# Performance work log

Measured on AMD Instinct MI355X. Metric: run time of the kernel, lower is better.

The kernel has to match this reference:

```python
import jax, jax.numpy as jnp
import numpy as np
import math

B, C, SEG, SEGLEN, K, GROUPS, WG = 8, 256, 40, 200, 10, 32, 4
L4 = SEGLEN // 4            # 50 temporal slots per segment
N = SEG * L4                # 2000 total points
WIDTH = GROUPS * WG         # 128 bottleneck width


def build_neighbor_idx(seg_lens):
    """Exact numpy replication of torch get_temporal_graph's neighbor-list loop.
    Returns flat (into B*N rows) neighbor indices of shape (B, N, 3)."""
    seg_lens = np.asarray(seg_lens)
    Bn, S = seg_lens.shape
    nb = np.zeros((Bn, S * L4, 3), dtype=np.int64)
    for i in range(Bn):
        last_valid = 0
        skip_seg = 0
        base = i * S * L4
        for j in range(S):
            valid = math.ceil(seg_lens[i, j] / 4.0)
            for k in range(L4):
                idx = j * L4 + k
                if k < valid:
                    nb[i, idx] = [base + last_valid, base + idx, base + idx]
                    last_valid = idx
                    if k == 0 and j != 0:
                        nb[i, skip_seg, 2] = base + idx
                    if k == valid - 1:
                        skip_seg = idx
                    else:
                        nb[i, idx, 2] = base + idx + 1
                else:
                    nb[i, idx] = [base + idx] * 3
    return nb


def conv1x1(x, W, b):
    # x: (B, Cin, N, T), W: (Cout, Cin)
    return jnp.einsum('bcnt,oc->bont', x, W) + b[None, :, None, None]


def grouped_1x3(x, W, b):
    # x: (B, WIDTH, N, 3), W: (WIDTH, WIDTH//GROUPS, 3); valid conv -> T_out = 1
    Bn, _, Nn, _ = x.shape
    xg = x.reshape(Bn, GROUPS, WIDTH // GROUPS, Nn, 3)
    Wg = W.reshape(GROUPS, WIDTH // GROUPS, WIDTH // GROUPS, 3)
    y = jnp.einsum('bgcnt,goct->bgon', xg, Wg)
    return y.reshape(Bn, WIDTH, Nn, 1) + b[None, :, None, None]


def grouped_1x1(x, W, b):
    # x: (B, WIDTH, N, T), W: (WIDTH, WIDTH//GROUPS)
    Bn, _, Nn, T = x.shape
    xg = x.reshape(Bn, GROUPS, WIDTH // GROUPS, Nn, T)
    Wg = W.reshape(GROUPS, WIDTH // GROUPS, WIDTH // GROUPS)
    y = jnp.einsum('bgcnt,goc->bgont', xg, Wg)
    return y.reshape(Bn, WIDTH, Nn, T) + b[None, :, None, None]


def setup_inputs() -> dict:
    key = jax.random.key(0)
    ks = jax.random.split(key, 10)
    s = 0.05
    x = jax.random.normal(ks[0], (B, C, N), dtype=jnp.float32)
    seg_lens = jax.random.randint(ks[1], (B, SEG), 0, 201)
    neighbor_idx = jnp.asarray(build_neighbor_idx(np.asarray(seg_lens)))
    return dict(
        x=x, seg_lens=seg_lens, neighbor_idx=neighbor_idx,
        tW1=jax.random.normal(ks[2], (WIDTH, C), jnp.float32) * s,
        tb1=jnp.zeros((WIDTH,), jnp.float32),
        tW2=jax.random.normal(ks[3], (WIDTH, WIDTH // GROUPS, 3), jnp.float32) * s,
        tb2=jnp.zeros((WIDTH,), jnp.float32),
        tW3=jax.random.normal(ks[4], (C, WIDTH), jnp.float32) * s,
        tb3=jnp.zeros((C,), jnp.float32),
        sW1=jax.random.normal(ks[5], (WIDTH, 2 * C), jnp.float32) * s,
        sb1=jnp.zeros((WIDTH,), jnp.float32),
        sW2=jax.random.normal(ks[6], (WIDTH, WIDTH // GROUPS), jnp.float32) * s,
        sb2=jnp.zeros((WIDTH,), jnp.float32),
        sW3=jax.random.normal(ks[7], (C, WIDTH), jnp.float32) * s,
        sb3=jnp.zeros((C,), jnp.float32),
    )


def reference(x, seg_lens, neighbor_idx, tW1, tb1, tW2, tb2, tW3, tb3,
              sW1, sb1, sW2, sb2, sW3, sb3):
    relu = jax.nn.relu
    B_, C_, N_ = x.shape
    flat = x.transpose(0, 2, 1).reshape(B_ * N_, C_)  # (B*N, C)

    # --- temporal branch: gather 3 temporal-graph neighbors -> (B, C, N, 3) ---
    tg = flat[neighbor_idx.reshape(-1)].reshape(B_, N_, 3, C_).transpose(0, 3, 1, 2)
    h = relu(conv1x1(tg, tW1, tb1))
    h = relu(grouped_1x3(h, tW2, tb2))
    tout = conv1x1(h, tW3, tb3).max(axis=-1)  # (B, C, N)

    # --- semantic branch: kNN graph feature (style=1) ---
    xx = jnp.sum(x * x, axis=1)                       # (B, N)
    inner = jnp.einsum('bci,bcj->bij', x, x)          # (B, N, N)
    pd = 2.0 * inner - xx[:, None, :] - xx[:, :, None]  # negative sq. distances
    _, idx = jax.lax.top_k(pd, K)                     # (B, N, K)
    base = (jnp.arange(B_) * N_)[:, None, None]
    nbr = flat[(idx + base).reshape(-1)].reshape(B_, N_, K, C_)
    center = jnp.broadcast_to(x.transpose(0, 2, 1)[:, :, None, :], (B_, N_, K, C_))
    xf = jnp.concatenate([nbr, center], axis=3).transpose(0, 3, 1, 2)  # (B, 2C, N, K)
    g = relu(conv1x1(xf, sW1, sb1))
    g = relu(grouped_1x1(g, sW2, sb2))
    sout = conv1x1(g, sW3, sb3).max(axis=-1)  # (B, C, N)

    return relu(tout + x + sout)
```

## Files before the change

kernel.cpp:

```cpp
#include <hip/hip_runtime.h>

#define NPTS 2000
#define NBATCH 8
#define NC 256
#define NW 128
#define NK 10
#define NROWS (NBATCH * NPTS)
#define JPAD 2048

typedef _Float16 f16x8 __attribute__((ext_vector_type(8)));
typedef _Float16 f16x4 __attribute__((ext_vector_type(4)));
typedef float f32x4 __attribute__((ext_vector_type(4)));

__device__ __forceinline__ float dot4(float4 a, float4 b) {
    return a.x*b.x + a.y*b.y + a.z*b.z + a.w*b.w;
}
__device__ __forceinline__ float4 relu4(float4 a) {
    return make_float4(fmaxf(a.x,0.f), fmaxf(a.y,0.f), fmaxf(a.z,0.f), fmaxf(a.w,0.f));
}
__device__ __forceinline__ float4 add4(float4 a, float4 b) {
    return make_float4(a.x+b.x, a.y+b.y, a.z+b.z, a.w+b.w);
}

__device__ __forceinline__ void ins10(float d, int j, float* vals, int* idxs) {
    if (d > vals[9]) {
        float v = d; int id = j;
        #pragma unroll
        for (int s = 0; s < 10; ++s) {
            if (v > vals[s]) {
                float tv = vals[s]; vals[s] = v; v = tv;
                int   ti = idxs[s]; idxs[s] = id; id = ti;
            }
        }
    }
}

__device__ __forceinline__ void gl_lds16(const void* g, void* l) {
    __builtin_amdgcn_global_load_lds(
        (const __attribute__((address_space(1))) void*)g,
        (__attribute__((address_space(3))) void*)l, 16, 0, 0);
}

__global__ __launch_bounds__(256) void k_prep(
    const float* __restrict__ x, _Float16* __restrict__ xb,
    float* __restrict__ xx)
{
    __shared__ float T[64][259];
    __shared__ float Pp[64][4];
    const int t  = threadIdx.x;
    const int b  = blockIdx.x >> 5;
    const int n0 = (blockIdx.x & 31) * 64;

    #pragma unroll
    for (int p = 0; p < 64; ++p) {
        const int idx = p*256 + t;
        const int c = idx >> 6, nl = idx & 63;
        T[nl][c] = x[((size_t)b*NC + c)*NPTS + min(n0 + nl, NPTS-1)];
    }
    __syncthreads();

    const int row = t & 63, q = t >> 6;
    const int gr  = n0 + row;
    const bool ok = gr < NPTS;
    const int sx  = gr & 7;
    float ss = 0.f;
    #pragma unroll
    for (int u = 0; u < 2; ++u) {
        const int kc = 2*q + u;
        const size_t base = ((size_t)(b*8 + kc)*JPAD + gr) * 64;
        #pragma unroll
        for (int g = 0; g < 4; ++g) {
            f16x8 vh, vl;
            #pragma unroll
            for (int e = 0; e < 8; ++e) {
                const float f = ok ? T[row][kc*32 + g*8 + e] : 0.f;
                ss = fmaf(f, f, ss);
                const _Float16 h = (_Float16)f;
                vh[e] = h;
                vl[e] = (_Float16)(f - (float)h);
            }
            *(f16x8*)&xb[base + (size_t)((g     ^ sx))*8] = vh;
            *(f16x8*)&xb[base + (size_t)(((4|g) ^ sx))*8] = vl;
        }
    }
    Pp[row][q] = ss;
    __syncthreads();
    if (t < 64 && n0 + t < NPTS)
        xx[(size_t)b*NPTS + n0 + t] = Pp[t][0] + Pp[t][1] + Pp[t][2] + Pp[t][3];
}

__global__ __launch_bounds__(256) void k_wprep(const float* __restrict__ a,
                                               _Float16* __restrict__ o, int n)
{
    const int i = (blockIdx.x*256 + threadIdx.x)*4;
    if (i < n) {
        const float4 v = *(const float4*)&a[i];
        f16x4 h = {(_Float16)v.x, (_Float16)v.y, (_Float16)v.z, (_Float16)v.w};
        *(f16x4*)&o[i] = h;
    }
}

__global__ __launch_bounds__(256) void k_wcat(
    const float* __restrict__ tW1, const float* __restrict__ sW1,
    _Float16* __restrict__ whcat)
{
    const int idx = blockIdx.x*256 + threadIdx.x;
    const int n = idx >> 8, k = idx & 255;
    float v;
    if (n < 128)      v = tW1[n*256 + k];
    else if (n < 256) v = sW1[(n-128)*512 + k];
    else              v = sW1[(n-256)*512 + 256 + k];
    whcat[idx] = (_Float16)v;
}

__global__ __launch_bounds__(256) void k_rowmm(
    const _Float16* __restrict__ xb, const _Float16* __restrict__ whcat,
    const float* __restrict__ tb1, const float* __restrict__ sb1,
    float* __restrict__ T1r, float* __restrict__ P, float* __restrict__ Q)
{
    const int t = threadIdx.x, lane = t & 63, w = t >> 6;
    const int lr = lane & 15, rg = lane >> 4;
    const int r0 = blockIdx.x * 16;
    const int b  = r0 / NPTS, jr = r0 % NPTS;

    const int row = jr + lr;
    const int sx  = row & 7;
    f16x8 ah[8], al[8];
    #pragma unroll
    for (int kc = 0; kc < 8; ++kc) {
        const size_t base = ((size_t)(b*8 + kc)*JPAD + row) * 64;
        ah[kc] = *(const f16x8*)&xb[base + (size_t)((rg     ^ sx))*8];
        al[kc] = *(const f16x8*)&xb[base + (size_t)(((4|rg) ^ sx))*8];
    }

    #pragma unroll
    for (int nt = 0; nt < 6; ++nt) {
        const int n0 = (w*6 + nt) * 16;
        f32x4 acc = {0.f,0.f,0.f,0.f};
        #pragma unroll
        for (int kc = 0; kc < 8; ++kc) {
            const f16x8 bw = *(const f16x8*)&whcat[(size_t)(n0 + lr)*256 + kc*32 + rg*8];
            acc = __builtin_amdgcn_mfma_f32_16x16x32_f16(ah[kc], bw, acc, 0,0,0);
            acc = __builtin_amdgcn_mfma_f32_16x16x32_f16(al[kc], bw, acc, 0,0,0);
        }
        const int n = n0 + lr;
        float bias; bool dorelu; float* dst;
        if (n < 128)      { bias = tb1[n];     dorelu = true;  dst = T1r + (size_t)r0*NW + n; }
        else if (n < 256) { bias = 0.f;        dorelu = false; dst = P   + (size_t)r0*NW + (n-128); }
        else              { bias = sb1[n-256]; dorelu = false; dst = Q   + (size_t)r0*NW + (n-256); }
        #pragma unroll
        for (int q = 0; q < 4; ++q) {
            float v = acc[q] + bias;
            if (dorelu) v = fmaxf(v, 0.f);
            dst[(size_t)(rg*4 + q)*NW] = v;
        }
    }
}

__global__ __attribute__((amdgpu_flat_work_group_size(256,256), amdgpu_waves_per_eu(2,2)))
void k_dist(const _Float16* __restrict__ xb, const float* __restrict__ xx,
            float* __restrict__ pval, int* __restrict__ pidx)
{
    __shared__ __align__(16) char smem[65536];

    const int t    = threadIdx.x;
    const int b    = blockIdx.x & 7;
    const int ip   = (blockIdx.x >> 3) & 15;
    const int jp   = blockIdx.x >> 7;
    const int i0   = ip * 128;
    const int j0p  = jp * 128;
    const int lane = t & 63;
    const int w    = t >> 6;
    const int lr   = lane & 15, rg = lane >> 4;
    const char* xbb = (const char*)xb;
    const float* xxb = xx + (size_t)b * NPTS;

    f32x4 acc[2][8] = {};

    {
        const size_t gbase = (size_t)(b*8 + 0) * JPAD;
        const char* gi = xbb + (gbase + i0) * 128;
        const char* gj = xbb + (gbase + j0p) * 128;
        #pragma unroll
        for (int r2 = 0; r2 < 4; ++r2) {
            gl_lds16(gi + t*16 + r2*4096, smem + t*16 + r2*4096);
            gl_lds16(gj + t*16 + r2*4096, smem + 16384 + t*16 + r2*4096);
        }
    }
    __syncthreads();

    for (int kc = 0; kc < 8; ++kc) {
        const int buf = kc & 1;

        if (kc < 7) {
            const size_t gbase = (size_t)(b*8 + kc + 1) * JPAD;
            const char* gi = xbb + (gbase + i0) * 128;
            const char* gj = xbb + (gbase + j0p) * 128;
            char* li = smem + (buf ^ 1)*32768;
            #pragma unroll
            for (int r2 = 0; r2 < 4; ++r2) {
                gl_lds16(gi + t*16 + r2*4096, li + t*16 + r2*4096);
                gl_lds16(gj + t*16 + r2*4096, li + 16384 + t*16 + r2*4096);
            }
        }

        {
            const char* IB = smem + buf*32768;
            const char* JB = IB + 16384;
            f16x8 bhf[2], blf[2];
            #pragma unroll
            for (int it = 0; it < 2; ++it) {
                const int il = (w*2 + it)*16 + lr;
                const int sx = il & 7;
                bhf[it] = *(const f16x8*)(IB + il*128 + ((rg     ^ sx))*16);
                blf[it] = *(const f16x8*)(IB + il*128 + (((4|rg) ^ sx))*16);
            }
            #pragma unroll
            for (int jt = 0; jt < 8; ++jt) {
                const int jl = jt*16 + lr;
                const int sx = jl & 7;
                const f16x8 ajh = *(const f16x8*)(JB + jl*128 + ((rg     ^ sx))*16);
                const f16x8 ajl = *(const f16x8*)(JB + jl*128 + (((4|rg) ^ sx))*16);
                #pragma unroll
                for (int it = 0; it < 2; ++it) {
                    acc[it][jt] = __builtin_amdgcn_mfma_f32_16x16x32_f16(ajh, bhf[it], acc[it][jt], 0,0,0);
                    acc[it][jt] = __builtin_amdgcn_mfma_f32_16x16x32_f16(ajh, blf[it], acc[it][jt], 0,0,0);
                    acc[it][jt] = __builtin_amdgcn_mfma_f32_16x16x32_f16(ajl, bhf[it], acc[it][jt], 0,0,0);
                }
            }
        }
        __syncthreads();
    }

    float v0[10], v1[10]; int x0[10], x1[10];
    #pragma unroll
    for (int s = 0; s < 10; ++s) { v0[s]=v1[s]=-3.0e38f; x0[s]=x1[s]=0x7fffffff; }

    #pragma unroll
    for (int jt = 0; jt < 8; ++jt) {
        const int jg0 = j0p + jt*16 + rg*4;
        const f32x4 xv = *(const f32x4*)&xxb[min(jg0, NPTS-4)];
        {
            const float d0 = 2.f*acc[0][jt][0] - xv[0];
            const float d1 = 2.f*acc[0][jt][1] - xv[1];
            const float d2 = 2.f*acc[0][jt][2] - xv[2];
            const float d3 = 2.f*acc[0][jt][3] - xv[3];
            if (fmaxf(fmaxf(d0,d1), fmaxf(d2,d3)) > v0[9]) {
                if (jg0     < NPTS) ins10(d0, jg0,     v0, x0);
                if (jg0 + 1 < NPTS) ins10(d1, jg0 + 1, v0, x0);
                if (jg0 + 2 < NPTS) ins10(d2, jg0 + 2, v0, x0);
                if (jg0 + 3 < NPTS) ins10(d3, jg0 + 3, v0, x0);
            }
        }
        {
            const float d0 = 2.f*acc[1][jt][0] - xv[0];
            const float d1 = 2.f*acc[1][jt][1] - xv[1];
            const float d2 = 2.f*acc[1][jt][2] - xv[2];
            const float d3 = 2.f*acc[1][jt][3] - xv[3];
            if (fmaxf(fmaxf(d0,d1), fmaxf(d2,d3)) > v1[9]) {
                if (jg0     < NPTS) ins10(d0, jg0,     v1, x1);
                if (jg0 + 1 < NPTS) ins10(d1, jg0 + 1, v1, x1);
                if (jg0 + 2 < NPTS) ins10(d2, jg0 + 2, v1, x1);
                if (jg0 + 3 < NPTS) ins10(d3, jg0 + 3, v1, x1);
            }
        }
    }

    float* mval = (float*)smem;
    int*   midx = (int*)(smem + 20480);
    {
        const int g0 = (w*2 + 0)*16 + lr;
        const int g1 = (w*2 + 1)*16 + lr;
        #pragma unroll
        for (int s = 0; s < 10; ++s) {
            mval[(g0*4 + rg)*10 + s] = v0[s];  midx[(g0*4 + rg)*10 + s] = x0[s];
            mval[(g1*4 + rg)*10 + s] = v1[s];  midx[(g1*4 + rg)*10 + s] = x1[s];
        }
    }
    __syncthreads();
    {
        const int g = t >> 1, pr = t & 1;
        float* va = &mval[(g*4 + pr)*10];     int* ia = &midx[(g*4 + pr)*10];
        const float* vb = &mval[(g*4 + pr + 2)*10]; const int* ib = &midx[(g*4 + pr + 2)*10];
        float ov[10]; int oi[10]; int pa = 0, pb = 0;
        #pragma unroll
        for (int s = 0; s < 10; ++s) {
            const float A = va[pa], Bv = vb[pb];
            const int  Ai = ia[pa], Bi = ib[pb];
            const bool ta = (A > Bv) || (A == Bv && Ai < Bi);
            ov[s] = ta ? A : Bv; oi[s] = ta ? Ai : Bi;
            pa += ta ? 1 : 0; pb += ta ? 0 : 1;
        }
        #pragma unroll
        for (int s = 0; s < 10; ++s) { va[s] = ov[s]; ia[s] = oi[s]; }
    }
    __syncthreads();
    if (t < 128) {
        const int g = t;
        const int ig = i0 + g;
        if (ig < NPTS) {
            const float* va = &mval[(g*4 + 0)*10]; const int* ia = &midx[(g*4 + 0)*10];
            const float* vb = &mval[(g*4 + 1)*10]; const int* ib = &midx[(g*4 + 1)*10];
            float* ov = &pval[((size_t)(b*NPTS + ig)*16 + jp)*10];
            int*   oi = &pidx[((size_t)(b*NPTS + ig)*16 + jp)*10];
            int pa = 0, pb = 0;
            #pragma unroll
            for (int s = 0; s < 10; ++s) {
                const float A = va[pa], Bv = vb[pb];
                const int  Ai = ia[pa], Bi = ib[pb];
                const bool ta = (A > Bv) || (A == Bv && Ai < Bi);
                ov[s] = ta ? A : Bv; oi[s] = ta ? Ai : Bi;
                pa += ta ? 1 : 0; pb += ta ? 0 : 1;
            }
        }
    }
}

__global__ __launch_bounds__(256) void k_tkm1(
    const float* __restrict__ pval, const int* __restrict__ pidx,
    float* __restrict__ pval2, int* __restrict__ pidx2)
{
    const int idx = blockIdx.x*256 + threadIdx.x;
    if (idx >= NROWS*4) return;
    const int r = idx >> 2, qt = idx & 3;
    const float* v  = &pval[((size_t)r*16 + qt*4)*10];
    const int*   ix = &pidx[((size_t)r*16 + qt*4)*10];
    float* ov = &pval2[(size_t)idx*10];
    int*   oi = &pidx2[(size_t)idx*10];
    int p0 = 0, p1 = 0, p2 = 0, p3 = 0;
    #pragma unroll
    for (int s = 0; s < NK; ++s) {
        float bv = -3.4e38f; int bi = 0x7fffffff; int bl = 0;
        { const float vv = v[p0];      const int ii = ix[p0];
          if (vv > bv || (vv == bv && ii < bi)) { bv = vv; bi = ii; bl = 0; } }
        { const float vv = v[10 + p1]; const int ii = ix[10 + p1];
          if (vv > bv || (vv == bv && ii < bi)) { bv = vv; bi = ii; bl = 1; } }
        { const float vv = v[20 + p2]; const int ii = ix[20 + p2];
          if (vv > bv || (vv == bv && ii < bi)) { bv = vv; bi = ii; bl = 2; } }
        { const float vv = v[30 + p3]; const int ii = ix[30 + p3];
          if (vv > bv || (vv == bv && ii < bi)) { bv = vv; bi = ii; bl = 3; } }
        p0 += (bl == 0); p1 += (bl == 1); p2 += (bl == 2); p3 += (bl == 3);
        ov[s] = bv; oi[s] = bi;
    }
}

__global__ __launch_bounds__(256) void k_tkm2(
    const float* __restrict__ pval2, const int* __restrict__ pidx2,
    int* __restrict__ tk)
{
    const int r = blockIdx.x*256 + threadIdx.x;
    if (r >= NROWS) return;
    const float* v  = &pval2[(size_t)r*40];
    const int*   ix = &pidx2[(size_t)r*40];
    const int base = (r / NPTS) * NPTS;
    int* op = &tk[(size_t)r*NK];
    int p0 = 0, p1 = 0, p2 = 0, p3 = 0;
    #pragma unroll
    for (int s = 0; s < NK; ++s) {
        float bv = -3.4e38f; int bi = 0x7fffffff; int bl = 0;
        { const float vv = v[p0];      const int ii = ix[p0];
          if (vv > bv || (vv == bv && ii < bi)) { bv = vv; bi = ii; bl = 0; } }
        { const float vv = v[10 + p1]; const int ii = ix[10 + p1];
          if (vv > bv || (vv == bv && ii < bi)) { bv = vv; bi = ii; bl = 1; } }
        { const float vv = v[20 + p2]; const int ii = ix[20 + p2];
          if (vv > bv || (vv == bv && ii < bi)) { bv = vv; bi = ii; bl = 2; } }
        { const float vv = v[30 + p3]; const int ii = ix[30 + p3];
          if (vv > bv || (vv == bv && ii < bi)) { bv = vv; bi = ii; bl = 3; } }
        p0 += (bl == 0); p1 += (bl == 1); p2 += (bl == 2); p3 += (bl == 3);
        op[s] = base + bi;
    }
}

#define AST 136
__global__ __launch_bounds__(256, 2) void k_fused(
    const float* __restrict__ x,
    const int* __restrict__ nb, const int* __restrict__ tk,
    const float* __restrict__ T1r, const float* __restrict__ P, const float* __restrict__ Q,
    const float* __restrict__ tW2, const float* __restrict__ tb2,
    const float* __restrict__ sW2, const float* __restrict__ sb2,
    const _Float16* __restrict__ wt3h, const _Float16* __restrict__ ws3h,
    const float* __restrict__ tb3, const float* __restrict__ sb3,
    float* __restrict__ out)
{
    __shared__ __align__(16) _Float16 A16[144*AST];
    __shared__ float Ssm[8][260];
    __shared__ float Zr[8][260];

    const int t  = threadIdx.x;
    const int r0 = blockIdx.x * 8;
    const int bb = r0 / NPTS;
    const int n0 = r0 % NPTS;

    {
        const float4 z4 = make_float4(0.f,0.f,0.f,0.f);
        float4* p4 = (float4*)A16;
        #pragma unroll
        for (int i = 0; i < 10; ++i) {
            const int idx = t + i*256;
            if (idx < 2448) p4[idx] = z4;
        }
    }
    __syncthreads();

    {
        const int o    = t & 127;
        const int half = t >> 7;
        const int g4   = o & ~3;

        const float4 f0 = *(const float4*)&tW2[o*12];
        const float4 f1 = *(const float4*)&tW2[o*12 + 4];
        const float4 f2 = *(const float4*)&tW2[o*12 + 8];
        const float4 wt0 = make_float4(f0.x, f0.w, f1.z, f2.y);
        const float4 wt1 = make_float4(f0.y, f1.x, f1.w, f2.z);
        const float4 wt2 = make_float4(f0.z, f1.y, f2.x, f2.w);
        const float4 wsw = *(const float4*)&sW2[o*4];
        const float tb2o = tb2[o], sb2o = sb2[o];

        #pragma unroll
        for (int ptl = 0; ptl < 4; ++ptl) {
            const int pt = half*4 + ptl;
            const int r  = r0 + pt;
            const int nb0 = nb[r*3+0], nb1 = nb[r*3+1], nb2 = nb[r*3+2];
            int ki[NK];
            #pragma unroll
            for (int k = 0; k < NK; ++k) ki[k] = tk[r*NK + k];
            const float4 h0 = *(const float4*)&T1r[(size_t)nb0*NW + g4];
            const float4 h1 = *(const float4*)&T1r[(size_t)nb1*NW + g4];
            const float4 h2 = *(const float4*)&T1r[(size_t)nb2*NW + g4];
            const float4 qf = *(const float4*)&Q[(size_t)r*NW + g4];
            float4 pf[NK];
            #pragma unroll
            for (int k = 0; k < NK; ++k) pf[k] = *(const float4*)&P[(size_t)ki[k]*NW + g4];

            const float z = tb2o + dot4(wt0,h0) + dot4(wt1,h1) + dot4(wt2,h2);
            A16[(128 + pt)*AST + o] = (_Float16)fmaxf(z, 0.f);
            #pragma unroll
            for (int k = 0; k < NK; ++k) {
                const float4 g1 = relu4(add4(pf[k], qf));
                A16[(pt*16 + k)*AST + o] = (_Float16)fmaxf(dot4(wsw, g1) + sb2o, 0.f);
            }
        }
    }
    __syncthreads();

    const int lane = t & 63, w = t >> 6;
    const int lr = lane & 15, lg = lane >> 4;
    const int n0w = w * 64;

    f32x4 accG[8][4] = {};
    f32x4 accZ[4] = {};

    #pragma unroll
    for (int kt = 0; kt < 4; ++kt) {
        const int ko = kt*32 + lg*8;
        f16x8 bs[4], bt[4];
        #pragma unroll
        for (int nt = 0; nt < 4; ++nt) {
            const int n = n0w + nt*16 + lr;
            bs[nt] = *(const f16x8*)&ws3h[n*NW + ko];
            bt[nt] = *(const f16x8*)&wt3h[n*NW + ko];
        }
        #pragma unroll
        for (int mt = 0; mt < 8; ++mt) {
            const f16x8 a = *(const f16x8*)&A16[(mt*16 + lr)*AST + ko];
            #pragma unroll
            for (int nt = 0; nt < 4; ++nt)
                accG[mt][nt] = __builtin_amdgcn_mfma_f32_16x16x32_f16(a, bs[nt], accG[mt][nt], 0,0,0);
        }
        const f16x8 az = *(const f16x8*)&A16[(128 + lr)*AST + ko];
        #pragma unroll
        for (int nt = 0; nt < 4; ++nt)
            accZ[nt] = __builtin_amdgcn_mfma_f32_16x16x32_f16(az, bt[nt], accZ[nt], 0,0,0);
    }

    const int rg = lg;
    #pragma unroll
    for (int mt = 0; mt < 8; ++mt) {
        #pragma unroll
        for (int nt = 0; nt < 4; ++nt) {
            float v;
            if (rg < 2)       v = fmaxf(fmaxf(accG[mt][nt][0], accG[mt][nt][1]),
                                        fmaxf(accG[mt][nt][2], accG[mt][nt][3]));
            else if (rg == 2) v = fmaxf(accG[mt][nt][0], accG[mt][nt][1]);
            else              v = -3.0e38f;
            v = fmaxf(v, __shfl_xor(v, 16));
            v = fmaxf(v, __shfl_xor(v, 32));
            if (lane < 16) Ssm[mt][n0w + nt*16 + lane] = v;
        }
    }
    #pragma unroll
    for (int nt = 0; nt < 4; ++nt) {
        #pragma unroll
        for (int q = 0; q < 4; ++q) {
            if (rg < 2) Zr[rg*4 + q][n0w + nt*16 + lr] = accZ[nt][q];
        }
    }
    __syncthreads();

    {
        const int c = t;
        const float tb = tb3[c], sb = sb3[c];
        const size_t go = ((size_t)bb*NC + c)*NPTS + n0;
        const float4 xv0 = *(const float4*)&x[go];
        const float4 xv1 = *(const float4*)&x[go + 4];
        const float xr[8] = {xv0.x,xv0.y,xv0.z,xv0.w, xv1.x,xv1.y,xv1.z,xv1.w};
        float ov[8];
        #pragma unroll
        for (int p = 0; p < 8; ++p)
            ov[p] = fmaxf(Zr[p][c] + tb + Ssm[p][c] + sb + xr[p], 0.f);
        *(float4*)&out[go]     = make_float4(ov[0],ov[1],ov[2],ov[3]);
        *(float4*)&out[go + 4] = make_float4(ov[4],ov[5],ov[6],ov[7]);
    }
}

extern "C" void kernel_launch(void* const* d_in, const int* in_sizes, int n_in,
                              void* d_out, int out_size, void* d_ws, size_t ws_size,
                              hipStream_t stream) {
    (void)in_sizes; (void)n_in; (void)out_size; (void)ws_size;
    const float* x   = (const float*)d_in[0];
    const int*   nb  = (const int*)d_in[2];
    const float* tW1 = (const float*)d_in[3];
    const float* tb1 = (const float*)d_in[4];
    const float* tW2 = (const float*)d_in[5];
    const float* tb2 = (const float*)d_in[6];
    const float* tW3 = (const float*)d_in[7];
    const float* tb3 = (const float*)d_in[8];
    const float* sW1 = (const float*)d_in[9];
    const float* sb1 = (const float*)d_in[10];
    const float* sW2 = (const float*)d_in[11];
    const float* sb2 = (const float*)d_in[12];
    const float* sW3 = (const float*)d_in[13];
    const float* sb3 = (const float*)d_in[14];
    float* out = (float*)d_out;

    float* ws  = (float*)d_ws;
    float* T1r   = ws;
    float* P     = ws + 2048000;
    float* Q     = ws + 4096000;
    float* xxp   = ws + 6144000;
    int*   tk    = (int*)(ws + 6160000);
    float* pval  = ws + 6320000;
    int*   pidx  = (int*)(ws + 8880000);
    float* pval2 = ws + 11440000;
    int*   pidx2 = (int*)(ws + 12080000);
    _Float16* xb    = (_Float16*)(ws + 12720000);
    _Float16* whcat = xb + (size_t)NBATCH * 8 * JPAD * 64;
    _Float16* wt3h  = whcat + 384 * 256;
    _Float16* ws3h  = wt3h + NC * NW;

    k_prep<<<NBATCH * 32, 256, 0, stream>>>(x, xb, xxp);
    k_wcat<<<384, 256, 0, stream>>>(tW1, sW1, whcat);
    k_wprep<<<32, 256, 0, stream>>>(tW3, wt3h, NC * NW);
    k_wprep<<<32, 256, 0, stream>>>(sW3, ws3h, NC * NW);
    k_rowmm<<<NROWS / 16, 256, 0, stream>>>(xb, whcat, tb1, sb1, T1r, P, Q);
    k_dist<<<2048, 256, 0, stream>>>(xb, xxp, pval, pidx);
    k_tkm1<<<(NROWS*4 + 255) / 256, 256, 0, stream>>>(pval, pidx, pval2, pidx2);
    k_tkm2<<<(NROWS + 255) / 256, 256, 0, stream>>>(pval2, pidx2, tk);
    k_fused<<<NROWS / 8, 256, 0, stream>>>(x, nb, tk, T1r, P, Q,
                                           tW2, tb2, sW2, sb2, wt3h, ws3h, tb3, sb3, out);
}
```

Before: 390.9 us.

## Stage distance tile through LDS and run top-10 selection per row-half

The k_dist epilogue now writes MFMA accumulators to a padded LDS buffer and reads them back so each thread scans 32 contiguous columns of one row. Previously each thread held two sets of 10-entry top-k lists in registers across the scattered MFMA output layout. The xx norms are also staged in LDS. This is meant to cut register pressure from the two live top-10 lists and give a more regular selection scan, at the cost of extra LDS traffic and several more block barriers. The launch attribute changes to __launch_bounds__(256, 2).

Measured after the change: 390.8 us. About the same (-0.0%).

```diff
diff --git a/kernel.cpp b/kernel.cpp
--- a/kernel.cpp
+++ b/kernel.cpp
@@ -157,11 +157,12 @@
     }
 }
 
-__global__ __attribute__((amdgpu_flat_work_group_size(256,256), amdgpu_waves_per_eu(2,2)))
+__global__ __launch_bounds__(256, 2)
 void k_dist(const _Float16* __restrict__ xb, const float* __restrict__ xx,
             float* __restrict__ pval, int* __restrict__ pidx)
 {
-    __shared__ __align__(16) char smem[65536];
+    __shared__ __align__(16) char smem[66048];
+    float* xxs = (float*)(smem + 65536);
 
     const int t    = threadIdx.x;
     const int b    = blockIdx.x & 7;
@@ -173,7 +174,8 @@
     const int w    = t >> 6;
     const int lr   = lane & 15, rg = lane >> 4;
     const char* xbb = (const char*)xb;
-    const float* xxb = xx + (size_t)b * NPTS;
+
+    if (t < 128) xxs[t] = xx[(size_t)b*NPTS + min(j0p + t, NPTS-1)];
 
     f32x4 acc[2][8] = {};
 
@@ -232,78 +234,54 @@
         __syncthreads();
     }
 
-    float v0[10], v1[10]; int x0[10], x1[10];
-    #pragma unroll
-    for (int s = 0; s < 10; ++s) { v0[s]=v1[s]=-3.0e38f; x0[s]=x1[s]=0x7fffffff; }
-
-    #pragma unroll
-    for (int jt = 0; jt < 8; ++jt) {
-        const int jg0 = j0p + jt*16 + rg*4;
-        const f32x4 xv = *(const f32x4*)&xxb[min(jg0, NPTS-4)];
+    float* Sbuf = (float*)smem;
+    float* mval = (float*)(smem + 34816);
+    int*   midx = (int*)(smem + 45056);
+
+    #pragma unroll
+    for (int it = 0; it < 2; ++it) {
+        #pragma unroll
+        for (int jt = 0; jt < 8; ++jt)
+            *(f32x4*)&Sbuf[(w*16 + lr)*132 + jt*16 + rg*4] = acc[it][jt];
+        __syncthreads();
+
+        float vv[10]; int xi[10];
+        #pragma unroll
+        for (int s = 0; s < 10; ++s) { vv[s] = -3.0e38f; xi[s] = 0x7fffffff; }
         {
-            const float d0 = 2.f*acc[0][jt][0] - xv[0];
-            const float d1 = 2.f*acc[0][jt][1] - xv[1];
-            const float d2 = 2.f*acc[0][jt][2] - xv[2];
-            const float d3 = 2.f*acc[0][jt][3] - xv[3];
-            if (fmaxf(fmaxf(d0,d1), fmaxf(d2,d3)) > v0[9]) {
-                if (jg0     < NPTS) ins10(d0, jg0,     v0, x0);
-                if (jg0 + 1 < NPTS) ins10(d1, jg0 + 1, v0, x0);
-                if (jg0 + 2 < NPTS) ins10(d2, jg0 + 2, v0, x0);
-                if (jg0 + 3 < NPTS) ins10(d3, jg0 + 3, v0, x0);
-            }
-        }
+            const int row = t & 63, jc = t >> 6;
+            const float* srow = &Sbuf[row*132 + jc*32];
+            #pragma unroll
+            for (int e4 = 0; e4 < 8; ++e4) {
+                const int jl = jc*32 + e4*4;
+                const int jg = j0p + jl;
+                const f32x4 sv = *(const f32x4*)&srow[e4*4];
+                const f32x4 xv = *(const f32x4*)&xxs[jl];
+                const float d0 = 2.f*sv[0] - xv[0];
+                const float d1 = 2.f*sv[1] - xv[1];
+                const float d2 = 2.f*sv[2] - xv[2];
+                const float d3 = 2.f*sv[3] - xv[3];
+                if (fmaxf(fmaxf(d0,d1), fmaxf(d2,d3)) > vv[9]) {
+                    if (jg     < NPTS) ins10(d0, jg,     vv, xi);
+                    if (jg + 1 < NPTS) ins10(d1, jg + 1, vv, xi);
+                    if (jg + 2 < NPTS) ins10(d2, jg + 2, vv, xi);
+                    if (jg + 3 < NPTS) ins10(d3, jg + 3, vv, xi);
+                }
+            }
+        }
+        __syncthreads();
         {
-            const float d0 = 2.f*acc[1][jt][0] - xv[0];
-            const float d1 = 2.f*acc[1][jt][1] - xv[1];
-            const float d2 = 2.f*acc[1][jt][2] - xv[2];
-            const float d3 = 2.f*acc[1][jt][3] - xv[3];
-            if (fmaxf(fmaxf(d0,d1), fmaxf(d2,d3)) > v1[9]) {
-                if (jg0     < NPTS) ins10(d0, jg0,     v1, x1);
-                if (jg0 + 1 < NPTS) ins10(d1, jg0 + 1, v1, x1);
-                if (jg0 + 2 < NPTS) ins10(d2, jg0 + 2, v1, x1);
-                if (jg0 + 3 < NPTS) ins10(d3, jg0 + 3, v1, x1);
-            }
-        }
-    }
-
-    float* mval = (float*)smem;
-    int*   midx = (int*)(smem + 20480);
-    {
-        const int g0 = (w*2 + 0)*16 + lr;
-        const int g1 = (w*2 + 1)*16 + lr;
-        #pragma unroll
-        for (int s = 0; s < 10; ++s) {
-            mval[(g0*4 + rg)*10 + s] = v0[s];  midx[(g0*4 + rg)*10 + s] = x0[s];
-            mval[(g1*4 + rg)*10 + s] = v1[s];  midx[(g1*4 + rg)*10 + s] = x1[s];
-        }
-    }
-    __syncthreads();
-    {
-        const int g = t >> 1, pr = t & 1;
-        float* va = &mval[(g*4 + pr)*10];     int* ia = &midx[(g*4 + pr)*10];
-        const float* vb = &mval[(g*4 + pr + 2)*10]; const int* ib = &midx[(g*4 + pr + 2)*10];
-        float ov[10]; int oi[10]; int pa = 0, pb = 0;
-        #pragma unroll
-        for (int s = 0; s < 10; ++s) {
-            const float A = va[pa], Bv = vb[pb];
-            const int  Ai = ia[pa], Bi = ib[pb];
-            const bool ta = (A > Bv) || (A == Bv && Ai < Bi);
-            ov[s] = ta ? A : Bv; oi[s] = ta ? Ai : Bi;
-            pa += ta ? 1 : 0; pb += ta ? 0 : 1;
-        }
-        #pragma unroll
-        for (int s = 0; s < 10; ++s) { va[s] = ov[s]; ia[s] = oi[s]; }
-    }
-    __syncthreads();
-    if (t < 128) {
-        const int g = t;
-        const int ig = i0 + g;
-        if (ig < NPTS) {
-            const float* va = &mval[(g*4 + 0)*10]; const int* ia = &midx[(g*4 + 0)*10];
-            const float* vb = &mval[(g*4 + 1)*10]; const int* ib = &midx[(g*4 + 1)*10];
-            float* ov = &pval[((size_t)(b*NPTS + ig)*16 + jp)*10];
-            int*   oi = &pidx[((size_t)(b*NPTS + ig)*16 + jp)*10];
-            int pa = 0, pb = 0;
+            const int row = t & 63, jc = t >> 6;
+            const int base = (row*4 + jc)*10;
+            #pragma unroll
+            for (int s = 0; s < 10; ++s) { mval[base+s] = vv[s]; midx[base+s] = xi[s]; }
+        }
+        __syncthreads();
+        if (t < 128) {
+            const int g = t >> 1, pr = t & 1;
+            float* va = &mval[(g*4 + pr)*10];     int* ia = &midx[(g*4 + pr)*10];
+            const float* vb = &mval[(g*4 + pr + 2)*10]; const int* ib = &midx[(g*4 + pr + 2)*10];
+            float ov[10]; int oi[10]; int pa = 0, pb = 0;
             #pragma unroll
             for (int s = 0; s < 10; ++s) {
                 const float A = va[pa], Bv = vb[pb];
@@ -312,7 +290,30 @@
                 ov[s] = ta ? A : Bv; oi[s] = ta ? Ai : Bi;
                 pa += ta ? 1 : 0; pb += ta ? 0 : 1;
             }
-        }
+            #pragma unroll
+            for (int s = 0; s < 10; ++s) { va[s] = ov[s]; ia[s] = oi[s]; }
+        }
+        __syncthreads();
+        if (t < 64) {
+            const int g = t;
+            const int ig = i0 + (g >> 4)*32 + it*16 + (g & 15);
+            if (ig < NPTS) {
+                const float* va = &mval[(g*4 + 0)*10]; const int* ia = &midx[(g*4 + 0)*10];
+                const float* vb = &mval[(g*4 + 1)*10]; const int* ib = &midx[(g*4 + 1)*10];
+                float* ov = &pval[((size_t)(b*NPTS + ig)*16 + jp)*10];
+                int*   oi = &pidx[((size_t)(b*NPTS + ig)*16 + jp)*10];
+                int pa = 0, pb = 0;
+                #pragma unroll
+                for (int s = 0; s < 10; ++s) {
+                    const float A = va[pa], Bv = vb[pb];
+                    const int  Ai = ia[pa], Bi = ib[pb];
+                    const bool ta = (A > Bv) || (A == Bv && Ai < Bi);
+                    ov[s] = ta ? A : Bv; oi[s] = ta ? Ai : Bi;
+                    pa += ta ? 1 : 0; pb += ta ? 0 : 1;
+                }
+            }
+        }
+        __syncthreads();
     }
 }
 
```
